# Kernel tuning notes

Measured on AMD Instinct MI355X. Metric: run time of the kernel, lower is better.

Reference implementation:

```python
import jax, jax.numpy as jnp
import numpy as np

N, Z_DIM = 131072, 64
K_CODES = 2048
QUANT_TEMP = 0.0  # default T when 'quant_temp' not passed


def setup_inputs() -> dict:
    key = jax.random.key(0)
    k1, k2 = jax.random.split(key)
    z = jax.random.normal(k1, (N, Z_DIM), dtype=jnp.float32)
    e = jax.random.normal(k2, (K_CODES, Z_DIM), dtype=jnp.float32)
    return {"z": z, "e": e}


def reference(z, e):
    # torch.cdist -> euclidean distance matrix [N, K]; argmin over squared
    # distance gives identical indices (sqrt is monotone), so skip the sqrt.
    # ||z - e||^2 = ||z||^2 - 2 z.e^T + ||e||^2
    z_sq = jnp.sum(z * z, axis=1, keepdims=True)          # [N, 1]
    e_sq = jnp.sum(e * e, axis=1)                          # [K]
    d2 = z_sq - 2.0 * (z @ e.T) + e_sq[None, :]            # [N, K]
    min_indices = jnp.argmin(d2, axis=1)                   # [N] int
    z_q = e[min_indices]                                   # gather [N, Z]
    commit_loss = jnp.mean((z - z_q) ** 2)                 # F.mse_loss
    # straight-through: z + (1 - T) * stop_grad(z_q - z), T = 0
    z_out = z + (1.0 - QUANT_TEMP) * jax.lax.stop_gradient(z_q - z)
    return z_out, min_indices, commit_loss
```

## Files before the change

### kernel.cpp

```cpp
#include <hip/hip_runtime.h>


#define N_ROWS 131072
#define ZD 64
#define KCODES 2048
#define RF 4
#define EPS_S 0.03f
#define FLAG_CAP 65536

using f16x8   = __attribute__((ext_vector_type(8))) _Float16;
using floatx4 = __attribute__((ext_vector_type(4))) float;


__global__ void prep_kernel(const float* __restrict__ e, float* __restrict__ ws) {
    int t = threadIdx.x, lane = t & 63, w = t >> 6;
    if (blockIdx.x == 0 && t == 0) { ws[0] = 0.0f; ((unsigned int*)ws)[1] = 0u; }
    int c = blockIdx.x * 4 + w;
    float* esn = ws + 1024;
    double* esq64 = (double*)((char*)ws + 16384);
    unsigned short* et = (unsigned short*)((char*)ws + 32768);
    float* eT = (float*)((char*)ws + 557056);

    float x = e[(size_t)c * ZD + lane];
    union { _Float16 h; unsigned short u; } cv;
    cv.h = (_Float16)x;
    int base = ((c >> 4) << 10) + ((lane >> 3) << 7) + ((c & 15) << 3) + (lane & 7);
    et[base] = cv.u;
    eT[lane * KCODES + c] = x;
    double s = (double)x * (double)x;
    for (int off = 1; off < 64; off <<= 1) s += __shfl_xor(s, off, 64);
    if (lane == 0) { esq64[c] = s; esn[c] = (float)(-0.5 * s); }
}

#define COMPUTE(H0, H1, EN, FCOL) do {                                       \
    floatx4 _ai = {EN, EN, EN, EN};                                          \
    _Pragma("unroll")                                                        \
    for (int _rf = 0; _rf < RF; _rf++) {                                     \
        floatx4 acc;                                                         \
        acc = __builtin_amdgcn_mfma_f32_16x16x32_f16(Fh[_rf][0], H0, _ai, 0, 0, 0); \
        acc = __builtin_amdgcn_mfma_f32_16x16x32_f16(Fh[_rf][1], H1, acc, 0, 0, 0); \
        _Pragma("unroll")                                                    \
        for (int _r = 0; _r < 4; _r++) {                                     \
            float _s  = acc[_r];                                             \
            bool  _gt = _s > mval[_rf][_r];                                  \
            mv2[_rf][_r]  = __builtin_amdgcn_fmed3f(_s, mval[_rf][_r], mv2[_rf][_r]); \
            midx[_rf][_r] = _gt ? (FCOL) : midx[_rf][_r];                    \
            mval[_rf][_r] = fmaxf(_s, mval[_rf][_r]);                        \
        }                                                                    \
    }                                                                        \
} while (0)

#define STAGEP(BUF, P) do {                                                  \
    const char* _src = etiles + ((size_t)((P) & 63) << 12)                   \
                       + ((size_t)threadIdx.x << 4);                         \
    __builtin_amdgcn_global_load_lds(                                        \
        (const __attribute__((address_space(1))) unsigned int*)_src,         \
        (__attribute__((address_space(3))) unsigned int*)&tilebuf[BUF][w << 10], \
        16, 0, 0);                                                           \
} while (0)

#define ITER2(BUF, P) do {                                                   \
    STAGEP((BUF) ^ 1, (P) + 1);                                              \
    float _en0 = esn_sm[(P) * 32 + lrow];                                    \
    float _en1 = esn_sm[(P) * 32 + 16 + lrow];                               \
    f16x8 h0, h1;                                                            \
    h0 = *(const f16x8*)(const void*)(tilebuf[BUF] + (lane << 4));           \
    h1 = *(const f16x8*)(const void*)(tilebuf[BUF] + 1024 + (lane << 4));    \
    COMPUTE(h0, h1, _en0, fcol);                                             \
    fcol += 16.0f;                                                           \
    h0 = *(const f16x8*)(const void*)(tilebuf[BUF] + 2048 + (lane << 4));    \
    h1 = *(const f16x8*)(const void*)(tilebuf[BUF] + 3072 + (lane << 4));    \
    COMPUTE(h0, h1, _en1, fcol);                                             \
    fcol += 16.0f;                                                           \
    __syncthreads();                                                         \
} while (0)

__global__ __launch_bounds__(256, 2) void vq_mfma(
        const float* __restrict__ z, const float* __restrict__ e,
        float* __restrict__ ws, float* __restrict__ out) {
    const char* etiles = (const char*)ws + 32768;
    unsigned int* cntp  = (unsigned int*)ws + 1;
    unsigned int* flags = (unsigned int*)((char*)ws + 294912);

    __shared__ __attribute__((aligned(16))) char tilebuf[2][4096];
    __shared__ __attribute__((aligned(16))) float esn_sm[KCODES];

    int lane = threadIdx.x & 63;
    int w    = threadIdx.x >> 6;
    int wid  = blockIdx.x * 4 + w;
    int row0 = wid * (RF * 16);
    int lrow = lane & 15;
    int lq   = lane >> 4;

    f16x8 Fh[RF][2];
#pragma unroll
    for (int rf = 0; rf < RF; rf++)
#pragma unroll
        for (int kc = 0; kc < 2; kc++) {
            const float* zp = z + (size_t)(row0 + rf * 16 + lrow) * ZD + kc * 32 + lq * 8;
            float xv[8];
            *(float4*)(void*)&xv[0] = *(const float4*)(const void*)zp;
            *(float4*)(void*)&xv[4] = *(const float4*)(const void*)(zp + 4);
            f16x8 h;
#pragma unroll
            for (int j = 0; j < 8; j++) h[j] = (_Float16)xv[j];
            Fh[rf][kc] = h;
            asm volatile("" : "+v"(Fh[rf][kc]));
        }

    {
        const char* esrc = (const char*)ws + 4096 + ((size_t)threadIdx.x << 4);
        __builtin_amdgcn_global_load_lds(
            (const __attribute__((address_space(1))) unsigned int*)esrc,
            (__attribute__((address_space(3))) unsigned int*)((char*)esn_sm + (w << 10)),
            16, 0, 0);
        __builtin_amdgcn_global_load_lds(
            (const __attribute__((address_space(1))) unsigned int*)(esrc + 4096),
            (__attribute__((address_space(3))) unsigned int*)((char*)esn_sm + 4096 + (w << 10)),
            16, 0, 0);
    }
    STAGEP(0, 0);

    floatx4 mval[RF], mv2[RF], midx[RF];
#pragma unroll
    for (int rf = 0; rf < RF; rf++)
#pragma unroll
        for (int r = 0; r < 4; r++) {
            mval[rf][r] = -3.0e38f; mv2[rf][r] = -3.0e38f; midx[rf][r] = 0.0f;
        }

    float fcol = (float)lrow;
    __syncthreads();

    for (int p = 0; p < 64; p += 2) {
        ITER2(0, p);
        ITER2(1, p + 1);
    }

    float lacc = 0.0f;
#pragma unroll
    for (int rf = 0; rf < RF; rf++)
#pragma unroll
        for (int r = 0; r < 4; r++) {
            float v = mval[rf][r], v2 = mv2[rf][r], fi = midx[rf][r];
            for (int off = 1; off < 16; off <<= 1) {
                float ov  = __shfl_xor(v,  off, 64);
                float ofi = __shfl_xor(fi, off, 64);
                float ov2 = __shfl_xor(v2, off, 64);
                bool take = (ov > v) || ((ov == v) && (ofi < fi));
                float loser = take ? v : ov;
                v2 = fmaxf(fmaxf(v2, ov2), loser);
                v  = take ? ov  : v;
                fi = take ? ofi : fi;
            }
            int row = row0 + rf * 16 + lq * 4 + r;
            int idx = (int)fi;
            float4 ev = ((const float4*)(const void*)(e + (size_t)idx * ZD))[lrow];
            float4 zv = ((const float4*)(const void*)(z + (size_t)row * ZD))[lrow];
            ((float4*)(void*)(out + (size_t)row * ZD))[lrow] = ev;
            float dx = ev.x - zv.x, dy = ev.y - zv.y;
            float dz = ev.z - zv.z, dw = ev.w - zv.w;
            lacc = fmaf(dx, dx, lacc); lacc = fmaf(dy, dy, lacc);
            lacc = fmaf(dz, dz, lacc); lacc = fmaf(dw, dw, lacc);
            if (lrow == 0) {
                out[(size_t)N_ROWS * ZD + row] = fi;
                if (v - v2 < EPS_S) {
                    unsigned int i = atomicAdd(cntp, 1u);
                    if (i < FLAG_CAP) flags[i] = (unsigned int)row;
                }
            }
        }

    for (int off = 1; off < 64; off <<= 1) lacc += __shfl_xor(lacc, off, 64);
    __shared__ float sm[4];
    if (lane == 0) sm[w] = lacc;
    __syncthreads();
    if (threadIdx.x == 0) atomicAdd(ws, sm[0] + sm[1] + sm[2] + sm[3]);
}

__global__ __launch_bounds__(256) void vq_fixup(
        const float* __restrict__ z, const float* __restrict__ e,
        float* __restrict__ ws, float* __restrict__ out) {
    const double* esq64 = (const double*)((const char*)ws + 16384);
    const float* eT = (const float*)((const char*)ws + 557056);
    const unsigned int* flags = (const unsigned int*)((const char*)ws + 294912);
    unsigned int cnt = ((const unsigned int*)ws)[1];
    bool allrows = cnt > FLAG_CAP;
    unsigned int n = allrows ? N_ROWS : cnt;

    if (blockIdx.x == 0 && threadIdx.x == 0)
        out[(size_t)N_ROWS * ZD + N_ROWS] = ws[0] * (1.0f / 8388608.0f);

    __shared__ float zrow[ZD];
    __shared__ double sd[4]; __shared__ int si[4]; __shared__ int sbest;
    int t = threadIdx.x, lane = t & 63, w = t >> 6;

    for (unsigned int u = blockIdx.x; u < n; u += gridDim.x) {
        int row = allrows ? (int)u : (int)flags[u];
        __syncthreads();
        if (t < ZD) zrow[t] = z[(size_t)row * ZD + t];
        __syncthreads();

        double dacc[8];
#pragma unroll
        for (int j = 0; j < 8; j++) dacc[j] = 0.0;
        for (int k = 0; k < ZD; k++) {
            double zk = (double)zrow[k];
            const float* ek = eT + k * KCODES + t;
#pragma unroll
            for (int j = 0; j < 8; j++)
                dacc[j] = fma(zk, (double)ek[256 * j], dacc[j]);
        }
        double dmin = 1.0e300; int imin = 0;
#pragma unroll
        for (int j = 0; j < 8; j++) {
            int c = t + 256 * j;
            double d = fma(-2.0, dacc[j], esq64[c]);
            if (d < dmin) { dmin = d; imin = c; }
        }
        for (int off = 1; off < 64; off <<= 1) {
            double od = __shfl_xor(dmin, off, 64);
            int    oi = __shfl_xor(imin, off, 64);
            if (od < dmin || (od == dmin && oi < imin)) { dmin = od; imin = oi; }
        }
        if (lane == 0) { sd[w] = dmin; si[w] = imin; }
        __syncthreads();
        if (t == 0) {
            double bd = sd[0]; int bi = si[0];
            for (int q = 1; q < 4; q++)
                if (sd[q] < bd || (sd[q] == bd && si[q] < bi)) { bd = sd[q]; bi = si[q]; }
            sbest = bi;
        }
        __syncthreads();
        int bi = sbest;
        if (t < 16)
            ((float4*)(void*)(out + (size_t)row * ZD))[t] =
                ((const float4*)(const void*)(e + (size_t)bi * ZD))[t];
        if (t == 0) out[(size_t)N_ROWS * ZD + row] = (float)bi;
    }
}

extern "C" void kernel_launch(void* const* d_in, const int* in_sizes, int n_in,
                              void* d_out, int out_size, void* d_ws, size_t ws_size,
                              hipStream_t stream) {
    const float* z = (const float*)d_in[0];
    const float* e = (const float*)d_in[1];
    float* out = (float*)d_out;
    float* ws  = (float*)d_ws;

    prep_kernel<<<dim3(512), dim3(256), 0, stream>>>(e, ws);
    vq_mfma<<<dim3(512), dim3(256), 0, stream>>>(z, e, ws, out);
    vq_fixup<<<dim3(1024), dim3(256), 0, stream>>>(z, e, ws, out);
}
```

Before: 203.3 us.

## Batch four flagged rows per fixup iteration and tighten the ambiguity margin

The fixup kernel now handles four flagged rows per block iteration. Each codebook column loaded from eT is reused across the four rows' fp64 FMAs, which cuts global/L2 traffic per row and amortizes the barriers. The ambiguity margin EPS_S is also lowered, so fewer rows should get flagged for exact fp64 recomputation. Risks: the narrower margin could miss near-ties that fp16 MFMA misranks, and the larger fp64 accumulator array raises register pressure.

Result: faster. 182.8 us (-10.1%).

```diff
diff --git a/kernel.cpp b/kernel.cpp
--- a/kernel.cpp
+++ b/kernel.cpp
@@ -5,8 +5,9 @@
 #define ZD 64
 #define KCODES 2048
 #define RF 4
-#define EPS_S 0.03f
+#define EPS_S 0.02f
 #define FLAG_CAP 65536
+#define RFIX 4
 
 using f16x8   = __attribute__((ext_vector_type(8))) _Float16;
 using floatx4 = __attribute__((ext_vector_type(4))) float;
@@ -190,53 +191,82 @@
 
     if (blockIdx.x == 0 && threadIdx.x == 0)
         out[(size_t)N_ROWS * ZD + N_ROWS] = ws[0] * (1.0f / 8388608.0f);
-
-    __shared__ float zrow[ZD];
-    __shared__ double sd[4]; __shared__ int si[4]; __shared__ int sbest;
+    if (n == 0) return;
+
+    __shared__ float zrow[RFIX][ZD];
+    __shared__ int rows_sm[RFIX];
+    __shared__ double sd[4][RFIX]; __shared__ int si[4][RFIX];
+    __shared__ int sbest[RFIX];
     int t = threadIdx.x, lane = t & 63, w = t >> 6;
 
-    for (unsigned int u = blockIdx.x; u < n; u += gridDim.x) {
-        int row = allrows ? (int)u : (int)flags[u];
-        __syncthreads();
-        if (t < ZD) zrow[t] = z[(size_t)row * ZD + t];
-        __syncthreads();
-
-        double dacc[8];
-#pragma unroll
-        for (int j = 0; j < 8; j++) dacc[j] = 0.0;
+    unsigned int ngroups = (n + RFIX - 1) / RFIX;
+    for (unsigned int g = blockIdx.x; g < ngroups; g += gridDim.x) {
+        __syncthreads();
+        if (t < RFIX) {
+            unsigned int u = g * RFIX + (unsigned int)t;
+            if (u >= n) u = n - 1;
+            rows_sm[t] = allrows ? (int)u : (int)flags[u];
+        }
+        __syncthreads();
+        zrow[t >> 6][t & 63] = z[(size_t)rows_sm[t >> 6] * ZD + (t & 63)];
+        __syncthreads();
+
+        double dacc[8][RFIX];
+#pragma unroll
+        for (int j = 0; j < 8; j++)
+#pragma unroll
+            for (int r = 0; r < RFIX; r++) dacc[j][r] = 0.0;
+
         for (int k = 0; k < ZD; k++) {
-            double zk = (double)zrow[k];
             const float* ek = eT + k * KCODES + t;
-#pragma unroll
-            for (int j = 0; j < 8; j++)
-                dacc[j] = fma(zk, (double)ek[256 * j], dacc[j]);
-        }
-        double dmin = 1.0e300; int imin = 0;
-#pragma unroll
-        for (int j = 0; j < 8; j++) {
-            int c = t + 256 * j;
-            double d = fma(-2.0, dacc[j], esq64[c]);
-            if (d < dmin) { dmin = d; imin = c; }
-        }
-        for (int off = 1; off < 64; off <<= 1) {
-            double od = __shfl_xor(dmin, off, 64);
-            int    oi = __shfl_xor(imin, off, 64);
-            if (od < dmin || (od == dmin && oi < imin)) { dmin = od; imin = oi; }
-        }
-        if (lane == 0) { sd[w] = dmin; si[w] = imin; }
-        __syncthreads();
-        if (t == 0) {
-            double bd = sd[0]; int bi = si[0];
+            float e8[8];
+#pragma unroll
+            for (int j = 0; j < 8; j++) e8[j] = ek[256 * j];
+#pragma unroll
+            for (int r = 0; r < RFIX; r++) {
+                double zk = (double)zrow[r][k];
+#pragma unroll
+                for (int j = 0; j < 8; j++)
+                    dacc[j][r] = fma(zk, (double)e8[j], dacc[j][r]);
+            }
+        }
+
+#pragma unroll
+        for (int r = 0; r < RFIX; r++) {
+            double dmin = 1.0e300; int imin = 0;
+#pragma unroll
+            for (int j = 0; j < 8; j++) {
+                int c = t + 256 * j;
+                double d = fma(-2.0, dacc[j][r], esq64[c]);
+                if (d < dmin) { dmin = d; imin = c; }
+            }
+            for (int off = 1; off < 64; off <<= 1) {
+                double od = __shfl_xor(dmin, off, 64);
+                int    oi = __shfl_xor(imin, off, 64);
+                if (od < dmin || (od == dmin && oi < imin)) { dmin = od; imin = oi; }
+            }
+            if (lane == 0) { sd[w][r] = dmin; si[w][r] = imin; }
+        }
+        __syncthreads();
+        if (t < RFIX) {
+            double bd = sd[0][t]; int bi = si[0][t];
             for (int q = 1; q < 4; q++)
-                if (sd[q] < bd || (sd[q] == bd && si[q] < bi)) { bd = sd[q]; bi = si[q]; }
-            sbest = bi;
-        }
-        __syncthreads();
-        int bi = sbest;
-        if (t < 16)
-            ((float4*)(void*)(out + (size_t)row * ZD))[t] =
-                ((const float4*)(const void*)(e + (size_t)bi * ZD))[t];
-        if (t == 0) out[(size_t)N_ROWS * ZD + row] = (float)bi;
+                if (sd[q][t] < bd || (sd[q][t] == bd && si[q][t] < bi)) {
+                    bd = sd[q][t]; bi = si[q][t];
+                }
+            sbest[t] = bi;
+        }
+        __syncthreads();
+        if (t < 16 * RFIX) {
+            int r = t >> 4, pos = t & 15;
+            unsigned int u = g * RFIX + (unsigned int)r;
+            if (u < n) {
+                int row = rows_sm[r]; int bi = sbest[r];
+                ((float4*)(void*)(out + (size_t)row * ZD))[pos] =
+                    ((const float4*)(const void*)(e + (size_t)bi * ZD))[pos];
+                if (pos == 0) out[(size_t)N_ROWS * ZD + row] = (float)bi;
+            }
+        }
     }
 }
 
```
